# Kernel optimization log

Hardware: AMD Instinct MI355X
Metric: run time of the kernel (lower is better)

Reference implementation:

```python
import jax, jax.numpy as jnp
import numpy as np

N_NODES = 50000
N_EDGES = 800000
D_IN = 128
D_OUT = 128


def setup_inputs() -> dict:
    key = jax.random.key(0)
    k_x, k_e, k_w, k_b = jax.random.split(key, 4)
    x = jax.random.normal(k_x, (N_NODES, D_IN), dtype=jnp.float32)
    edge_index = jax.random.randint(k_e, (2, N_EDGES), 0, N_NODES, dtype=jnp.int64)
    # nn.Linear(in_dim, out_dim): W is [out, in], b is [out]
    W = jax.random.normal(k_w, (D_OUT, D_IN), dtype=jnp.float32) * (1.0 / np.sqrt(D_IN))
    b = jax.random.normal(k_b, (D_OUT,), dtype=jnp.float32) * 0.01
    return {"x": x, "edge_index": edge_index, "W": W, "b": b}


def reference(x, edge_index, W, b):
    row, col = edge_index[0], edge_index[1]
    n = x.shape[0]
    # scatter-add of gathered source features: agg[row] += x[col]
    agg = jax.ops.segment_sum(x[col], row, num_segments=n)  # [N, d_in]
    # in-degree per destination node (bincount of row), clamped to >= 1
    deg = jax.ops.segment_sum(jnp.ones((row.shape[0],), dtype=x.dtype), row,
                              num_segments=n)
    deg = jnp.maximum(deg, 1.0)[:, None]  # [N, 1]
    agg = agg / deg
    # linear (y = agg @ W.T + b) then relu
    return jax.nn.relu(jnp.einsum('nd,od->no', agg, W) + b)
```

## Files before the change

### kernel.cpp

```cpp
#include <hip/hip_runtime.h>

#define N_NODES 50000
#define N_EDGES 800000
#define D 128

#define NCRS 196
#define CCAP 4608
#define EPB 2048
#define NEBLK ((N_EDGES + EPB - 1) / EPB)
#define NFB 1563
#define LCAP 1536
#define XN (N_NODES * D / 4)
#define WN (D * D / 4)
#define CVTBLK ((XN + WN + 255) / 256)

#define XB_OFF   0u
#define WB_OFF   12800000u
#define GCUR_OFF 12832768u
#define CRS_OFF  12833792u
#define WS_NEED_A (CRS_OFF + (unsigned)NCRS * CCAP * 4u)

#define CNT_OFF 0u
#define OFF_OFF 200704u
#define CUR_OFF 401920u
#define CSR_OFF 602112u
#define WT_OFF  3802112u
#define PART_OFF 3867648u
#define BASE_OFF 3868672u
#define WS_NEED_B (BASE_OFF + 1024u)

#define SCAN_B 256
#define SCAN_NBLK ((N_NODES + SCAN_B - 1) / SCAN_B)

using bf16x8 = __attribute__((ext_vector_type(8))) short;
using f32x4 = __attribute__((ext_vector_type(4))) float;

static __device__ __forceinline__ unsigned short bf16_rne(float f) {
  unsigned u = __float_as_uint(f);
  return (unsigned short)((u + 0x7fffu + ((u >> 16) & 1u)) >> 16);
}
static __device__ __forceinline__ unsigned pack_bf16(float a, float b) {
  return (unsigned)bf16_rne(a) | ((unsigned)bf16_rne(b) << 16);
}
static __device__ __forceinline__ float bf_lo(unsigned v) {
  return __uint_as_float(v << 16);
}
static __device__ __forceinline__ float bf_hi(unsigned v) {
  return __uint_as_float(v & 0xffff0000u);
}

__global__ __launch_bounds__(256) void zero_gcur(unsigned* __restrict__ gcur) {
  if (threadIdx.x < NCRS) gcur[threadIdx.x] = 0u;
}

__global__ __launch_bounds__(256) void phase1(
    const float4* __restrict__ x4, uint2* __restrict__ xb,
    const float4* __restrict__ w4, uint2* __restrict__ wb,
    const int* __restrict__ ei, unsigned* __restrict__ gcur,
    unsigned* __restrict__ crs) {
  const int t = threadIdx.x;

  if (blockIdx.x < NEBLK) {
    __shared__ unsigned ent[EPB];
    __shared__ unsigned srt[EPB];
    __shared__ unsigned s[256];
    __shared__ unsigned offx[NCRS], cur[NCRS], gb[NCRS];
    const int base = blockIdx.x * EPB;
    const int n = (N_EDGES - base < EPB) ? (N_EDGES - base) : EPB;
    for (int i = t; i < n; i += 256) {
      unsigned dst = (unsigned)ei[base + i];
      unsigned src = (unsigned)ei[N_EDGES + base + i];
      ent[i] = ((dst >> 8) << 24) | (src << 8) | (dst & 255u);
    }
    s[t] = 0;
    __syncthreads();
    for (int i = t; i < n; i += 256) atomicAdd(&s[ent[i] >> 24], 1u);
    __syncthreads();
    unsigned c = s[t];
    __syncthreads();
    s[t] = c;
    __syncthreads();
    #pragma unroll
    for (int o = 1; o < 256; o <<= 1) {
      unsigned a = (t >= o) ? s[t - o] : 0u;
      __syncthreads();
      s[t] += a;
      __syncthreads();
    }
    unsigned ex = s[t] - c;
    if (t < NCRS) {
      offx[t] = ex;
      cur[t] = ex;
      if (c) gb[t] = atomicAdd(&gcur[t], c);
    }
    __syncthreads();
    for (int i = t; i < n; i += 256) {
      unsigned e = ent[i];
      unsigned pos = atomicAdd(&cur[e >> 24], 1u);
      srt[pos] = e;
    }
    __syncthreads();
    for (int i = t; i < n; i += 256) {
      unsigned e = srt[i];
      unsigned k = e >> 24;
      unsigned idx = gb[k] + ((unsigned)i - offx[k]);
      if (idx < CCAP) crs[k * CCAP + idx] = e;
    }
  } else {
    int i = (blockIdx.x - NEBLK) * 256 + t;
    if (i < XN) {
      float4 v = x4[i];
      uint2 r;
      r.x = pack_bf16(v.x, v.y);
      r.y = pack_bf16(v.z, v.w);
      xb[i] = r;
    } else if (i < XN + WN) {
      int j = i - XN;
      float4 v = w4[j];
      uint2 r;
      r.x = pack_bf16(v.x, v.y);
      r.y = pack_bf16(v.z, v.w);
      wb[j] = r;
    }
  }
}

__global__ __launch_bounds__(256) void sortbins(
    const unsigned* __restrict__ gcur, unsigned* __restrict__ crs) {
  __shared__ unsigned ent[CCAP];
  __shared__ unsigned s[256], cur[256];
  const int t = threadIdx.x;
  const int c = blockIdx.x;
  unsigned n = gcur[c];
  n = (n > CCAP) ? CCAP : n;
  unsigned* region = crs + (unsigned)c * CCAP;

  for (unsigned i = t; i < n; i += 256) ent[i] = region[i];
  cur[t] = 0;
  __syncthreads();
  for (unsigned i = t; i < n; i += 256) atomicAdd(&cur[ent[i] & 255u], 1u);
  __syncthreads();
  unsigned cc = cur[t];
  __syncthreads();
  s[t] = cc;
  __syncthreads();
  #pragma unroll
  for (int o = 1; o < 256; o <<= 1) {
    unsigned a = (t >= o) ? s[t - o] : 0u;
    __syncthreads();
    s[t] += a;
    __syncthreads();
  }
  unsigned ex = s[t] - cc;
  unsigned* offs = region + 2304;
  offs[t] = ex;
  if (t == 255) offs[256] = n;
  cur[t] = ex;
  __syncthreads();
  unsigned short* lst = (unsigned short*)region;
  for (unsigned i = t; i < n; i += 256) {
    unsigned e = ent[i];
    unsigned pos = atomicAdd(&cur[e & 255u], 1u);
    lst[pos] = (unsigned short)((e >> 8) & 0xFFFFu);
  }
}

__global__ __launch_bounds__(256) void agg_gemm(
    const unsigned* __restrict__ xb, const unsigned short* __restrict__ wb,
    const unsigned* __restrict__ crs, const float* __restrict__ b,
    float* __restrict__ out) {
  __shared__ unsigned abuf[32 * 64];
  __shared__ unsigned short llst[LCAP];
  __shared__ unsigned loffs[33];
  const int t = threadIdx.x;
  const int fb = blockIdx.x;
  const int coarse = fb >> 3;
  const int ln0 = (fb & 7) * 32;

  const unsigned* region = crs + (unsigned)coarse * CCAP;
  const unsigned* offs = region + 2304;
  const unsigned short* lst = (const unsigned short*)region;

  if (t < 33) loffs[t] = offs[ln0 + t];
  __syncthreads();
  const unsigned base = loffs[0];
  unsigned total = loffs[32] - base;
  if (total > LCAP) total = LCAP;
  for (unsigned i = t; i < total; i += 256) llst[i] = lst[base + i];
  __syncthreads();

  const int stream = t >> 5;
  const int p2 = t & 31;
  const uint2* x2 = (const uint2*)xb;
  for (int r = stream; r < 32; r += 8) {
    unsigned beg = loffs[r] - base, end = loffs[r + 1] - base;
    float a0 = 0.f, a1 = 0.f, a2 = 0.f, a3 = 0.f;
    unsigned j = beg;
    for (; j + 8 <= end; j += 8) {
      uint2 v0 = x2[(size_t)llst[j] * 32 + p2];
      uint2 v1 = x2[(size_t)llst[j + 1] * 32 + p2];
      uint2 v2 = x2[(size_t)llst[j + 2] * 32 + p2];
      uint2 v3 = x2[(size_t)llst[j + 3] * 32 + p2];
      uint2 v4 = x2[(size_t)llst[j + 4] * 32 + p2];
      uint2 v5 = x2[(size_t)llst[j + 5] * 32 + p2];
      uint2 v6 = x2[(size_t)llst[j + 6] * 32 + p2];
      uint2 v7 = x2[(size_t)llst[j + 7] * 32 + p2];
      a0 += (bf_lo(v0.x) + bf_lo(v1.x)) + (bf_lo(v2.x) + bf_lo(v3.x)) +
            ((bf_lo(v4.x) + bf_lo(v5.x)) + (bf_lo(v6.x) + bf_lo(v7.x)));
      a1 += (bf_hi(v0.x) + bf_hi(v1.x)) + (bf_hi(v2.x) + bf_hi(v3.x)) +
            ((bf_hi(v4.x) + bf_hi(v5.x)) + (bf_hi(v6.x) + bf_hi(v7.x)));
      a2 += (bf_lo(v0.y) + bf_lo(v1.y)) + (bf_lo(v2.y) + bf_lo(v3.y)) +
            ((bf_lo(v4.y) + bf_lo(v5.y)) + (bf_lo(v6.y) + bf_lo(v7.y)));
      a3 += (bf_hi(v0.y) + bf_hi(v1.y)) + (bf_hi(v2.y) + bf_hi(v3.y)) +
            ((bf_hi(v4.y) + bf_hi(v5.y)) + (bf_hi(v6.y) + bf_hi(v7.y)));
    }
    for (; j + 2 <= end; j += 2) {
      uint2 v0 = x2[(size_t)llst[j] * 32 + p2];
      uint2 v1 = x2[(size_t)llst[j + 1] * 32 + p2];
      a0 += bf_lo(v0.x) + bf_lo(v1.x);
      a1 += bf_hi(v0.x) + bf_hi(v1.x);
      a2 += bf_lo(v0.y) + bf_lo(v1.y);
      a3 += bf_hi(v0.y) + bf_hi(v1.y);
    }
    if (j < end) {
      uint2 v = x2[(size_t)llst[j] * 32 + p2];
      a0 += bf_lo(v.x);
      a1 += bf_hi(v.x);
      a2 += bf_lo(v.y);
      a3 += bf_hi(v.y);
    }
    float inv = 1.0f / fmaxf((float)(end - beg), 1.0f);
    unsigned w0 = (unsigned)(2 * p2) ^ ((unsigned)(r & 7) << 2);
    *(uint2*)&abuf[r * 64 + w0] =
        make_uint2(pack_bf16(a0 * inv, a1 * inv), pack_bf16(a2 * inv, a3 * inv));
  }
  __syncthreads();

  const int wave = t >> 6, lane = t & 63;
  const int rt = wave >> 1;
  const int ch = (wave & 1) * 64;
  const int arow = lane & 15, khi = lane >> 4;
  const int ar = rt * 16 + arow;
  bf16x8 afrag[4];
  #pragma unroll
  for (int kb = 0; kb < 4; ++kb) {
    int w0 = (kb * 16 + khi * 4) ^ ((ar & 7) << 2);
    afrag[kb] = *(const bf16x8*)&abuf[ar * 64 + w0];
  }
  #pragma unroll
  for (int ct = 0; ct < 4; ++ct) {
    int o = ch + ct * 16 + arow;
    f32x4 acc = (f32x4){0.f, 0.f, 0.f, 0.f};
    #pragma unroll
    for (int kb = 0; kb < 4; ++kb) {
      bf16x8 bfrag = *(const bf16x8*)(wb + o * 128 + kb * 32 + khi * 8);
      acc = __builtin_amdgcn_mfma_f32_16x16x32_bf16(afrag[kb], bfrag, acc,
                                                    0, 0, 0);
    }
    float bias = b[o];
    #pragma unroll
    for (int rg = 0; rg < 4; ++rg) {
      int row = fb * 32 + rt * 16 + khi * 4 + rg;
      if (row < N_NODES)
        out[(size_t)row * 128 + o] = fmaxf(acc[rg] + bias, 0.0f);
    }
  }
}

__global__ __launch_bounds__(256) void transpose_w(
    const float* __restrict__ W, float* __restrict__ Wt) {
  int i = blockIdx.x * 256 + threadIdx.x;
  if (i < D * D) {
    int o = i >> 7, d = i & 127;
    Wt[d * D + o] = W[i];
  }
}

__global__ __launch_bounds__(256) void count_kernel(
    const int* __restrict__ ei, unsigned* __restrict__ cnt) {
  int e = blockIdx.x * 256 + threadIdx.x;
  if (e < N_EDGES) atomicAdd(&cnt[ei[e]], 1u);
}

__global__ __launch_bounds__(256) void scan_p1(
    const unsigned* __restrict__ cnt, unsigned* __restrict__ partial) {
  int t = threadIdx.x;
  int g = blockIdx.x * SCAN_B + t;
  unsigned c = (g < N_NODES) ? cnt[g] : 0u;
  #pragma unroll
  for (int o = 32; o > 0; o >>= 1) c += __shfl_down(c, o, 64);
  __shared__ unsigned ws[4];
  if ((t & 63) == 0) ws[t >> 6] = c;
  __syncthreads();
  if (t == 0) partial[blockIdx.x] = ws[0] + ws[1] + ws[2] + ws[3];
}

__global__ __launch_bounds__(256) void scan_p2(
    const unsigned* __restrict__ partial, unsigned* __restrict__ base,
    unsigned* __restrict__ off) {
  __shared__ unsigned s[256];
  int t = threadIdx.x;
  unsigned v = (t < SCAN_NBLK) ? partial[t] : 0u;
  s[t] = v;
  __syncthreads();
  #pragma unroll
  for (int o = 1; o < 256; o <<= 1) {
    unsigned a = (t >= o) ? s[t - o] : 0u;
    __syncthreads();
    s[t] += a;
    __syncthreads();
  }
  if (t < SCAN_NBLK) base[t] = s[t] - v;
  if (t == 255) off[N_NODES] = s[255];
}

__global__ __launch_bounds__(256) void scan_p3(
    const unsigned* __restrict__ cnt, const unsigned* __restrict__ base,
    unsigned* __restrict__ off, unsigned* __restrict__ cur) {
  __shared__ unsigned s[256];
  int t = threadIdx.x;
  int g = blockIdx.x * SCAN_B + t;
  unsigned c = (g < N_NODES) ? cnt[g] : 0u;
  s[t] = c;
  __syncthreads();
  #pragma unroll
  for (int o = 1; o < 256; o <<= 1) {
    unsigned a = (t >= o) ? s[t - o] : 0u;
    __syncthreads();
    s[t] += a;
    __syncthreads();
  }
  if (g < N_NODES) {
    unsigned e = base[blockIdx.x] + s[t] - c;
    off[g] = e;
    cur[g] = e;
  }
}

__global__ __launch_bounds__(256) void fill_kernel(
    const int* __restrict__ ei, unsigned* __restrict__ cur,
    int* __restrict__ csr) {
  int e = blockIdx.x * 256 + threadIdx.x;
  if (e < N_EDGES) {
    int dst = ei[e];
    int src = ei[N_EDGES + e];
    unsigned pos = atomicAdd(&cur[dst], 1u);
    csr[pos] = src;
  }
}

__global__ __launch_bounds__(256) void aggregate_kernel(
    const float* __restrict__ x, const unsigned* __restrict__ off,
    const int* __restrict__ csr, float* __restrict__ agg) {
  int wave = (blockIdx.x * 256 + threadIdx.x) >> 6;
  int lane = threadIdx.x & 63;
  if (wave >= N_NODES) return;
  unsigned beg = off[wave], end = off[wave + 1];
  const float2* x2 = (const float2*)x;
  float ax = 0.f, ay = 0.f;
  unsigned i = beg;
  for (; i + 2 <= end; i += 2) {
    int s0 = csr[i], s1 = csr[i + 1];
    float2 v0 = x2[(size_t)s0 * 64 + lane];
    float2 v1 = x2[(size_t)s1 * 64 + lane];
    ax += v0.x + v1.x;
    ay += v0.y + v1.y;
  }
  if (i < end) {
    float2 v = x2[(size_t)csr[i] * 64 + lane];
    ax += v.x;
    ay += v.y;
  }
  float inv = 1.0f / fmaxf((float)(end - beg), 1.0f);
  float2 r;
  r.x = ax * inv;
  r.y = ay * inv;
  ((float2*)agg)[(size_t)wave * 64 + lane] = r;
}

__global__ __launch_bounds__(256) void gemm_relu_kernel(
    float* __restrict__ io, const float* __restrict__ deg,
    const float* __restrict__ Wt, const float* __restrict__ b) {
  __shared__ float a_lds[32 * 128];
  int tid = threadIdx.x;
  int row0 = blockIdx.x * 32;
  const float4* g4 = (const float4*)io + (size_t)row0 * 32;
  #pragma unroll
  for (int k = 0; k < 4; ++k) {
    int f = k * 256 + tid;
    int r = f >> 5;
    int grow = row0 + r;
    float4 v = make_float4(0.f, 0.f, 0.f, 0.f);
    float inv = 1.0f;
    if (grow < N_NODES) {
      v = g4[f];
      if (deg) inv = 1.0f / fmaxf(deg[grow], 1.0f);
    }
    float* dstp = &a_lds[f * 4];
    dstp[0] = v.x * inv;
    dstp[1] = v.y * inv;
    dstp[2] = v.z * inv;
    dstp[3] = v.w * inv;
  }
  __syncthreads();
  int cq = tid & 31;
  int rb = (tid >> 5) * 4;
  float acc[4][4] = {};
  const float4* Wt4 = (const float4*)Wt;
  #pragma unroll 4
  for (int d = 0; d < 128; ++d) {
    float4 w = Wt4[d * 32 + cq];
    #pragma unroll
    for (int i = 0; i < 4; ++i) {
      float a = a_lds[(rb + i) * 128 + d];
      acc[i][0] += a * w.x;
      acc[i][1] += a * w.y;
      acc[i][2] += a * w.z;
      acc[i][3] += a * w.w;
    }
  }
  float4 bb = ((const float4*)b)[cq];
  float4* out4 = (float4*)io;
  #pragma unroll
  for (int i = 0; i < 4; ++i) {
    int grow = row0 + rb + i;
    if (grow < N_NODES) {
      float4 r;
      r.x = fmaxf(acc[i][0] + bb.x, 0.0f);
      r.y = fmaxf(acc[i][1] + bb.y, 0.0f);
      r.z = fmaxf(acc[i][2] + bb.z, 0.0f);
      r.w = fmaxf(acc[i][3] + bb.w, 0.0f);
      out4[(size_t)grow * 32 + cq] = r;
    }
  }
}

__global__ __launch_bounds__(256) void scatter_kernel(
    const float* __restrict__ x, const int* __restrict__ ei,
    float* __restrict__ agg, float* __restrict__ deg) {
  int gid = blockIdx.x * 256 + threadIdx.x;
  int e = gid >> 5;
  if (e >= N_EDGES) return;
  int part = gid & 31;
  int dst = ei[e];
  int src = ei[N_EDGES + e];
  const float4* x4 = (const float4*)x;
  float4 v = x4[(size_t)src * 32 + part];
  float* base = agg + (size_t)dst * D + part * 4;
  atomicAdd(base + 0, v.x);
  atomicAdd(base + 1, v.y);
  atomicAdd(base + 2, v.z);
  atomicAdd(base + 3, v.w);
  if (part == 0) atomicAdd(deg + dst, 1.0f);
}

extern "C" void kernel_launch(void* const* d_in, const int* in_sizes, int n_in,
                              void* d_out, int out_size, void* d_ws, size_t ws_size,
                              hipStream_t stream) {
  const float* x = (const float*)d_in[0];
  const int* ei = (const int*)d_in[1];
  const float* W = (const float*)d_in[2];
  const float* b = (const float*)d_in[3];
  float* out = (float*)d_out;

  if (ws_size >= WS_NEED_A) {
    unsigned* xb = (unsigned*)((char*)d_ws + XB_OFF);
    unsigned short* wb = (unsigned short*)((char*)d_ws + WB_OFF);
    unsigned* gcur = (unsigned*)((char*)d_ws + GCUR_OFF);
    unsigned* crs = (unsigned*)((char*)d_ws + CRS_OFF);

    zero_gcur<<<1, 256, 0, stream>>>(gcur);
    phase1<<<NEBLK + CVTBLK, 256, 0, stream>>>(
        (const float4*)x, (uint2*)xb, (const float4*)W, (uint2*)wb,
        ei, gcur, crs);
    sortbins<<<NCRS, 256, 0, stream>>>(gcur, crs);
    agg_gemm<<<NFB, 256, 0, stream>>>(xb, wb, crs, b, out);
  } else if (ws_size >= WS_NEED_B) {
    unsigned* cnt = (unsigned*)((char*)d_ws + CNT_OFF);
    unsigned* off = (unsigned*)((char*)d_ws + OFF_OFF);
    unsigned* cur = (unsigned*)((char*)d_ws + CUR_OFF);
    int* csr = (int*)((char*)d_ws + CSR_OFF);
    float* Wt = (float*)((char*)d_ws + WT_OFF);
    unsigned* partial = (unsigned*)((char*)d_ws + PART_OFF);
    unsigned* base = (unsigned*)((char*)d_ws + BASE_OFF);

    hipMemsetAsync(cnt, 0, N_NODES * sizeof(unsigned), stream);
    transpose_w<<<(D * D + 255) / 256, 256, 0, stream>>>(W, Wt);
    count_kernel<<<(N_EDGES + 255) / 256, 256, 0, stream>>>(ei, cnt);
    scan_p1<<<SCAN_NBLK, 256, 0, stream>>>(cnt, partial);
    scan_p2<<<1, 256, 0, stream>>>(partial, base, off);
    scan_p3<<<SCAN_NBLK, 256, 0, stream>>>(cnt, base, off, cur);
    fill_kernel<<<(N_EDGES + 255) / 256, 256, 0, stream>>>(ei, cur, csr);
    aggregate_kernel<<<(N_NODES * 64 + 255) / 256, 256, 0, stream>>>(
        x, off, csr, out);
    gemm_relu_kernel<<<(N_NODES + 31) / 32, 256, 0, stream>>>(
        out, nullptr, Wt, b);
  } else {
    float* deg = (float*)d_ws;
    float* Wt = (float*)((char*)d_ws + 256 * 1024);
    hipMemsetAsync(d_out, 0, (size_t)N_NODES * D * sizeof(float), stream);
    hipMemsetAsync(deg, 0, N_NODES * sizeof(float), stream);
    transpose_w<<<(D * D + 255) / 256, 256, 0, stream>>>(W, Wt);
    scatter_kernel<<<(N_EDGES * 32) / 256, 256, 0, stream>>>(x, ei, out, deg);
    gemm_relu_kernel<<<(N_NODES + 31) / 32, 256, 0, stream>>>(out, deg, Wt, b);
  }
}
```

Baseline: 75.21 us.

## Halve agg_gemm tile to 16 rows with 16-byte gathers and wave-shuffle scans

The aggregation+GEMM kernel now processes 16 destination rows per block instead of 32, doubling the block count. Each of 16 threads per row gathers 16-byte (8 bf16) chunks rather than 8-byte chunks, and each row gets its own thread group instead of streams looping over rows. The 256-wide block prefix scans in phase1 and sortbins are replaced by a wave-shuffle scan plus a small cross-wave sum, cutting many barriers. The row bound check in the output store is dropped, which relies on 3125*16 exactly covering the node count.

```diff
diff --git a/kernel.cpp b/kernel.cpp
--- a/kernel.cpp
+++ b/kernel.cpp
@@ -8,8 +8,8 @@
 #define CCAP 4608
 #define EPB 2048
 #define NEBLK ((N_EDGES + EPB - 1) / EPB)
-#define NFB 1563
-#define LCAP 1536
+#define NFB 3125
+#define LCAP16 768
 #define XN (N_NODES * D / 4)
 #define WN (D * D / 4)
 #define CVTBLK ((XN + WN + 255) / 256)
@@ -49,6 +49,23 @@
   return __uint_as_float(v & 0xffff0000u);
 }
 
+static __device__ __forceinline__ unsigned wave_excl_scan_256(
+    unsigned c, int t, unsigned* wsum) {
+  unsigned xinc = c;
+  #pragma unroll
+  for (int o = 1; o < 64; o <<= 1) {
+    unsigned n = __shfl_up(xinc, o, 64);
+    if ((t & 63) >= o) xinc += n;
+  }
+  if ((t & 63) == 63) wsum[t >> 6] = xinc;
+  __syncthreads();
+  unsigned add = 0;
+  #pragma unroll
+  for (int w = 0; w < 4; ++w)
+    if (w < (t >> 6)) add += wsum[w];
+  return xinc - c + add;
+}
+
 __global__ __launch_bounds__(256) void zero_gcur(unsigned* __restrict__ gcur) {
   if (threadIdx.x < NCRS) gcur[threadIdx.x] = 0u;
 }
@@ -64,6 +81,7 @@
     __shared__ unsigned ent[EPB];
     __shared__ unsigned srt[EPB];
     __shared__ unsigned s[256];
+    __shared__ unsigned wsum[4];
     __shared__ unsigned offx[NCRS], cur[NCRS], gb[NCRS];
     const int base = blockIdx.x * EPB;
     const int n = (N_EDGES - base < EPB) ? (N_EDGES - base) : EPB;
@@ -77,17 +95,7 @@
     for (int i = t; i < n; i += 256) atomicAdd(&s[ent[i] >> 24], 1u);
     __syncthreads();
     unsigned c = s[t];
-    __syncthreads();
-    s[t] = c;
-    __syncthreads();
-    #pragma unroll
-    for (int o = 1; o < 256; o <<= 1) {
-      unsigned a = (t >= o) ? s[t - o] : 0u;
-      __syncthreads();
-      s[t] += a;
-      __syncthreads();
-    }
-    unsigned ex = s[t] - c;
+    unsigned ex = wave_excl_scan_256(c, t, wsum);
     if (t < NCRS) {
       offx[t] = ex;
       cur[t] = ex;
@@ -128,7 +136,8 @@
 __global__ __launch_bounds__(256) void sortbins(
     const unsigned* __restrict__ gcur, unsigned* __restrict__ crs) {
   __shared__ unsigned ent[CCAP];
-  __shared__ unsigned s[256], cur[256];
+  __shared__ unsigned cur[256];
+  __shared__ unsigned wsum[4];
   const int t = threadIdx.x;
   const int c = blockIdx.x;
   unsigned n = gcur[c];
@@ -141,20 +150,11 @@
   for (unsigned i = t; i < n; i += 256) atomicAdd(&cur[ent[i] & 255u], 1u);
   __syncthreads();
   unsigned cc = cur[t];
-  __syncthreads();
-  s[t] = cc;
-  __syncthreads();
-  #pragma unroll
-  for (int o = 1; o < 256; o <<= 1) {
-    unsigned a = (t >= o) ? s[t - o] : 0u;
-    __syncthreads();
-    s[t] += a;
-    __syncthreads();
-  }
-  unsigned ex = s[t] - cc;
+  unsigned ex = wave_excl_scan_256(cc, t, wsum);
   unsigned* offs = region + 2304;
   offs[t] = ex;
   if (t == 255) offs[256] = n;
+  __syncthreads();
   cur[t] = ex;
   __syncthreads();
   unsigned short* lst = (unsigned short*)region;
@@ -169,42 +169,43 @@
     const unsigned* __restrict__ xb, const unsigned short* __restrict__ wb,
     const unsigned* __restrict__ crs, const float* __restrict__ b,
     float* __restrict__ out) {
-  __shared__ unsigned abuf[32 * 64];
-  __shared__ unsigned short llst[LCAP];
-  __shared__ unsigned loffs[33];
+  __shared__ unsigned abuf[16 * 64];
+  __shared__ unsigned short llst[LCAP16];
+  __shared__ unsigned loffs[17];
   const int t = threadIdx.x;
   const int fb = blockIdx.x;
-  const int coarse = fb >> 3;
-  const int ln0 = (fb & 7) * 32;
+  const int coarse = fb >> 4;
+  const int ln0 = (fb & 15) * 16;
 
   const unsigned* region = crs + (unsigned)coarse * CCAP;
   const unsigned* offs = region + 2304;
   const unsigned short* lst = (const unsigned short*)region;
 
-  if (t < 33) loffs[t] = offs[ln0 + t];
+  if (t < 17) loffs[t] = offs[ln0 + t];
   __syncthreads();
   const unsigned base = loffs[0];
-  unsigned total = loffs[32] - base;
-  if (total > LCAP) total = LCAP;
+  unsigned total = loffs[16] - base;
+  if (total > LCAP16) total = LCAP16;
   for (unsigned i = t; i < total; i += 256) llst[i] = lst[base + i];
   __syncthreads();
 
-  const int stream = t >> 5;
-  const int p2 = t & 31;
-  const uint2* x2 = (const uint2*)xb;
-  for (int r = stream; r < 32; r += 8) {
+  const int r = t >> 4;
+  const int p4 = t & 15;
+  const uint4* x4g = (const uint4*)xb;
+  {
     unsigned beg = loffs[r] - base, end = loffs[r + 1] - base;
     float a0 = 0.f, a1 = 0.f, a2 = 0.f, a3 = 0.f;
+    float a4 = 0.f, a5 = 0.f, a6 = 0.f, a7 = 0.f;
     unsigned j = beg;
     for (; j + 8 <= end; j += 8) {
-      uint2 v0 = x2[(size_t)llst[j] * 32 + p2];
-      uint2 v1 = x2[(size_t)llst[j + 1] * 32 + p2];
-      uint2 v2 = x2[(size_t)llst[j + 2] * 32 + p2];
-      uint2 v3 = x2[(size_t)llst[j + 3] * 32 + p2];
-      uint2 v4 = x2[(size_t)llst[j + 4] * 32 + p2];
-      uint2 v5 = x2[(size_t)llst[j + 5] * 32 + p2];
-      uint2 v6 = x2[(size_t)llst[j + 6] * 32 + p2];
-      uint2 v7 = x2[(size_t)llst[j + 7] * 32 + p2];
+      uint4 v0 = x4g[(size_t)llst[j] * 16 + p4];
+      uint4 v1 = x4g[(size_t)llst[j + 1] * 16 + p4];
+      uint4 v2 = x4g[(size_t)llst[j + 2] * 16 + p4];
+      uint4 v3 = x4g[(size_t)llst[j + 3] * 16 + p4];
+      uint4 v4 = x4g[(size_t)llst[j + 4] * 16 + p4];
+      uint4 v5 = x4g[(size_t)llst[j + 5] * 16 + p4];
+      uint4 v6 = x4g[(size_t)llst[j + 6] * 16 + p4];
+      uint4 v7 = x4g[(size_t)llst[j + 7] * 16 + p4];
       a0 += (bf_lo(v0.x) + bf_lo(v1.x)) + (bf_lo(v2.x) + bf_lo(v3.x)) +
             ((bf_lo(v4.x) + bf_lo(v5.x)) + (bf_lo(v6.x) + bf_lo(v7.x)));
       a1 += (bf_hi(v0.x) + bf_hi(v1.x)) + (bf_hi(v2.x) + bf_hi(v3.x)) +
@@ -213,43 +214,57 @@
             ((bf_lo(v4.y) + bf_lo(v5.y)) + (bf_lo(v6.y) + bf_lo(v7.y)));
       a3 += (bf_hi(v0.y) + bf_hi(v1.y)) + (bf_hi(v2.y) + bf_hi(v3.y)) +
             ((bf_hi(v4.y) + bf_hi(v5.y)) + (bf_hi(v6.y) + bf_hi(v7.y)));
+      a4 += (bf_lo(v0.z) + bf_lo(v1.z)) + (bf_lo(v2.z) + bf_lo(v3.z)) +
+            ((bf_lo(v4.z) + bf_lo(v5.z)) + (bf_lo(v6.z) + bf_lo(v7.z)));
+      a5 += (bf_hi(v0.z) + bf_hi(v1.z)) + (bf_hi(v2.z) + bf_hi(v3.z)) +
+            ((bf_hi(v4.z) + bf_hi(v5.z)) + (bf_hi(v6.z) + bf_hi(v7.z)));
+      a6 += (bf_lo(v0.w) + bf_lo(v1.w)) + (bf_lo(v2.w) + bf_lo(v3.w)) +
+            ((bf_lo(v4.w) + bf_lo(v5.w)) + (bf_lo(v6.w) + bf_lo(v7.w)));
+      a7 += (bf_hi(v0.w) + bf_hi(v1.w)) + (bf_hi(v2.w) + bf_hi(v3.w)) +
+            ((bf_hi(v4.w) + bf_hi(v5.w)) + (bf_hi(v6.w) + bf_hi(v7.w)));
     }
     for (; j + 2 <= end; j += 2) {
-      uint2 v0 = x2[(size_t)llst[j] * 32 + p2];
-      uint2 v1 = x2[(size_t)llst[j + 1] * 32 + p2];
+      uint4 v0 = x4g[(size_t)llst[j] * 16 + p4];
+      uint4 v1 = x4g[(size_t)llst[j + 1] * 16 + p4];
       a0 += bf_lo(v0.x) + bf_lo(v1.x);
       a1 += bf_hi(v0.x) + bf_hi(v1.x);
       a2 += bf_lo(v0.y) + bf_lo(v1.y);
       a3 += bf_hi(v0.y) + bf_hi(v1.y);
+      a4 += bf_lo(v0.z) + bf_lo(v1.z);
+      a5 += bf_hi(v0.z) + bf_hi(v1.z);
+      a6 += bf_lo(v0.w) + bf_lo(v1.w);
+      a7 += bf_hi(v0.w) + bf_hi(v1.w);
     }
     if (j < end) {
-      uint2 v = x2[(size_t)llst[j] * 32 + p2];
+      uint4 v = x4g[(size_t)llst[j] * 16 + p4];
       a0 += bf_lo(v.x);
       a1 += bf_hi(v.x);
       a2 += bf_lo(v.y);
       a3 += bf_hi(v.y);
+      a4 += bf_lo(v.z);
+      a5 += bf_hi(v.z);
+      a6 += bf_lo(v.w);
+      a7 += bf_hi(v.w);
     }
     float inv = 1.0f / fmaxf((float)(end - beg), 1.0f);
-    unsigned w0 = (unsigned)(2 * p2) ^ ((unsigned)(r & 7) << 2);
-    *(uint2*)&abuf[r * 64 + w0] =
-        make_uint2(pack_bf16(a0 * inv, a1 * inv), pack_bf16(a2 * inv, a3 * inv));
+    unsigned w0 = (unsigned)(4 * p4) ^ ((unsigned)(r & 7) << 2);
+    *(uint4*)&abuf[r * 64 + w0] =
+        make_uint4(pack_bf16(a0 * inv, a1 * inv), pack_bf16(a2 * inv, a3 * inv),
+                   pack_bf16(a4 * inv, a5 * inv), pack_bf16(a6 * inv, a7 * inv));
   }
   __syncthreads();
 
   const int wave = t >> 6, lane = t & 63;
-  const int rt = wave >> 1;
-  const int ch = (wave & 1) * 64;
   const int arow = lane & 15, khi = lane >> 4;
-  const int ar = rt * 16 + arow;
   bf16x8 afrag[4];
   #pragma unroll
   for (int kb = 0; kb < 4; ++kb) {
-    int w0 = (kb * 16 + khi * 4) ^ ((ar & 7) << 2);
-    afrag[kb] = *(const bf16x8*)&abuf[ar * 64 + w0];
-  }
-  #pragma unroll
-  for (int ct = 0; ct < 4; ++ct) {
-    int o = ch + ct * 16 + arow;
+    int w0 = (kb * 16 + khi * 4) ^ ((arow & 7) << 2);
+    afrag[kb] = *(const bf16x8*)&abuf[arow * 64 + w0];
+  }
+  #pragma unroll
+  for (int ct = 0; ct < 2; ++ct) {
+    int o = wave * 32 + ct * 16 + arow;
     f32x4 acc = (f32x4){0.f, 0.f, 0.f, 0.f};
     #pragma unroll
     for (int kb = 0; kb < 4; ++kb) {
@@ -260,9 +275,8 @@
     float bias = b[o];
     #pragma unroll
     for (int rg = 0; rg < 4; ++rg) {
-      int row = fb * 32 + rt * 16 + khi * 4 + rg;
-      if (row < N_NODES)
-        out[(size_t)row * 128 + o] = fmaxf(acc[rg] + bias, 0.0f);
+      int row = fb * 16 + khi * 4 + rg;
+      out[(size_t)row * 128 + o] = fmaxf(acc[rg] + bias, 0.0f);
     }
   }
 }
```

Result: faster. 70.46 us (-6.3%).
